# Kernel optimization log

Hardware: AMD Instinct MI355X
Metric: run time of the kernel (lower is better)

Reference implementation:

```python
import jax, jax.numpy as jnp
import numpy as np

EPS = 1e-5

def layer_norm(x, g, b):
    mu = jnp.mean(x, axis=-1, keepdims=True)
    var = jnp.var(x, axis=-1, keepdims=True)
    return (x - mu) * jax.lax.rsqrt(var + EPS) * g + b

def setup_inputs() -> dict:
    key = jax.random.key(0)
    ks = jax.random.split(key, 12)
    B, N, D, H = 32, 577, 768, 12
    Dh = D // H
    hid = 4 * D
    s = lambda d: 1.0 / np.sqrt(d)
    return {
        "x": jax.random.normal(ks[0], (B, N, D), jnp.float32),
        "ln1_g": jnp.ones((D,), jnp.float32),
        "ln1_b": jnp.zeros((D,), jnp.float32),
        "ln2_g": jnp.ones((D,), jnp.float32),
        "ln2_b": jnp.zeros((D,), jnp.float32),
        "w_qkv": jax.random.normal(ks[1], (D, 3 * D), jnp.float32) * s(D),
        "b_qkv": jnp.zeros((3 * D,), jnp.float32),
        "w_proj": jax.random.normal(ks[2], (D, D), jnp.float32) * s(D),
        "b_proj": jnp.zeros((D,), jnp.float32),
        "w_fc1": jax.random.normal(ks[3], (D, hid), jnp.float32) * s(D),
        "b_fc1": jnp.zeros((hid,), jnp.float32),
        "w_fc2": jax.random.normal(ks[4], (hid, D), jnp.float32) * s(hid),
        "b_fc2": jnp.zeros((D,), jnp.float32),
    }

def reference(x, ln1_g, ln1_b, ln2_g, ln2_b, w_qkv, b_qkv, w_proj, b_proj,
              w_fc1, b_fc1, w_fc2, b_fc2):
    B, N, D = x.shape
    H = 12
    Dh = D // H
    scale = Dh ** -0.5
    # --- attention branch ---
    h = layer_norm(x, ln1_g, ln1_b)
    qkv = h @ w_qkv + b_qkv                      # [B, N, 3D]
    qkv = qkv.reshape(B, N, 3, H, Dh).transpose(2, 0, 3, 1, 4)  # [3, B, H, N, Dh]
    q, k, v = qkv[0], qkv[1], qkv[2]
    attn = jnp.einsum('bhnd,bhmd->bhnm', q, k) * scale  # [B, H, N, N]
    attn = jax.nn.softmax(attn, axis=-1)
    o = jnp.einsum('bhnm,bhmd->bhnd', attn, v)           # [B, H, N, Dh]
    o = o.transpose(0, 2, 1, 3).reshape(B, N, D)
    o = o @ w_proj + b_proj
    x = x + o
    # --- MLP branch ---
    h = layer_norm(x, ln2_g, ln2_b)
    h = jnp.clip(h @ w_fc1 + b_fc1, 0.0, 6.0)            # ReLU6
    h = h @ w_fc2 + b_fc2
    return x + h
```

## Files before the change

kernel.cpp:

```cpp
#include <hip/hip_runtime.h>
#include <math.h>


typedef unsigned short u16;
typedef _Float16 f16;
typedef __attribute__((ext_vector_type(8))) _Float16 f16x8;
typedef __attribute__((ext_vector_type(4))) float f32x4;

__device__ __forceinline__ u16 f2h(float x) {
    union { f16 h; u16 u; } cv;
    cv.h = (f16)x;
    return cv.u;
}
__device__ __forceinline__ float h2f(u16 b) {
    union { u16 u; f16 h; } cv;
    cv.u = b;
    return (float)cv.h;
}
__device__ __forceinline__ void load_lds16(const u16* g, void* l) {
    __builtin_amdgcn_global_load_lds(
        (const __attribute__((address_space(1))) void*)g,
        (__attribute__((address_space(3))) void*)l, 16, 0, 0);
}
__device__ __forceinline__ int xcd_swz(int lid, int nwg) {
    const int x = lid & 7, pos = lid >> 3;
    const int q = nwg >> 3, r = nwg & 7;
    return (x < r ? x * (q + 1) : r * (q + 1) + (x - r) * q) + pos;
}

__global__ __launch_bounds__(256)
void wprep_kernel(const float* __restrict__ W, u16* __restrict__ Th,
                  int K, int N)
{
    __shared__ float t[32][33];
    const int n0 = blockIdx.x * 32, k0 = blockIdx.y * 32;
    const int tr = threadIdx.x >> 3, tc4 = (threadIdx.x & 7) * 4;
    const float4 v = *(const float4*)&W[(size_t)(k0 + tr) * N + n0 + tc4];
    t[tr][tc4 + 0] = v.x; t[tr][tc4 + 1] = v.y;
    t[tr][tc4 + 2] = v.z; t[tr][tc4 + 3] = v.w;
    __syncthreads();
    ushort4 h;
    h.x = f2h(t[tc4 + 0][tr]);
    h.y = f2h(t[tc4 + 1][tr]);
    h.z = f2h(t[tc4 + 2][tr]);
    h.w = f2h(t[tc4 + 3][tr]);
    *(ushort4*)&Th[(size_t)(n0 + tr) * K + k0 + tc4] = h;
}

__global__ __launch_bounds__(256)
void ln_kernel(const float* __restrict__ x, const float* __restrict__ g,
               const float* __restrict__ beta, u16* __restrict__ oh)
{
    const int row = blockIdx.x;
    const int tid = threadIdx.x;
    const float* xr = x + (size_t)row * 768;
    const float v0 = xr[tid], v1 = xr[tid + 256], v2 = xr[tid + 512];
    float s  = v0 + v1 + v2;
    float ss = v0 * v0 + v1 * v1 + v2 * v2;
    #pragma unroll
    for (int off = 1; off < 64; off <<= 1) {
        s  += __shfl_xor(s, off);
        ss += __shfl_xor(ss, off);
    }
    __shared__ float redS[4], redQ[4];
    const int wid = tid >> 6;
    if ((tid & 63) == 0) { redS[wid] = s; redQ[wid] = ss; }
    __syncthreads();
    s  = redS[0] + redS[1] + redS[2] + redS[3];
    ss = redQ[0] + redQ[1] + redQ[2] + redQ[3];
    const float mean = s * (1.0f / 768.0f);
    const float var  = ss * (1.0f / 768.0f) - mean * mean;
    const float rstd = rsqrtf(var + 1e-5f);
    u16* ohr = oh + (size_t)row * 768;
    #pragma unroll
    for (int u = 0; u < 3; ++u) {
        const int c = tid + u * 256;
        const float vv = (u == 0) ? v0 : (u == 1) ? v1 : v2;
        ohr[c] = f2h((vv - mean) * rstd * g[c] + beta[c]);
    }
}

template<int RELU6, int RES, int OMODE>
__global__ __launch_bounds__(256)
void mfma_gemm(const u16* __restrict__ Ah, const u16* __restrict__ Bh,
               const float* __restrict__ bias, const float* res,
               float* Cf, u16* __restrict__ Ch,
               u16* __restrict__ Qh_, u16* __restrict__ Kh_,
               u16* __restrict__ Vth_,
               int M, int N, int K)
{
    constexpr int LDSN = (OMODE == 2) ? 17408 : 16384;
    __shared__ u16 lds[LDSN];

    const int tid  = threadIdx.x;
    const int wave = tid >> 6;
    const int lane = tid & 63;

    const int nwg = gridDim.x * gridDim.y;
    int lid = blockIdx.y * gridDim.x + blockIdx.x;
    lid = xcd_swz(lid, nwg);
    const int bm = (lid / gridDim.x) * 128;
    const int bn = (lid % gridDim.x) * 128;

    const int r0 = wave * 16 + (lane >> 2);
    const int r1 = 64 + r0;
    const int c  = lane & 3;
    const int kg0 = c ^ ((r0 >> 1) & 3);
    const int kg1 = c ^ ((r1 >> 1) & 3);

    const u16* pA0 = Ah + (size_t)(bm + r0) * K + 8 * kg0;
    const u16* pA1 = Ah + (size_t)(bm + r1) * K + 8 * kg1;
    const u16* pB0 = Bh + (size_t)(bn + r0) * K + 8 * kg0;
    const u16* pB1 = Bh + (size_t)(bn + r1) * K + 8 * kg1;

    char* ldsb = (char*)lds;
    char* dA0 = ldsb +     0 + wave * 1024;
    char* dA1 = ldsb +  4096 + wave * 1024;
    char* dB0 = ldsb +  8192 + wave * 1024;
    char* dB1 = ldsb + 12288 + wave * 1024;

    const int am0 = (wave >> 1) * 64;
    const int bn0 = (wave & 1) * 64;
    const int l15 = lane & 15;
    const int lg  = lane >> 4;

    f32x4 acc[4][4] = {};
    const int nk = K >> 5;

    load_lds16(pA0, dA0); load_lds16(pA1, dA1);
    load_lds16(pB0, dB0); load_lds16(pB1, dB1);
    pA0 += 32; pA1 += 32; pB0 += 32; pB1 += 32;
    __syncthreads();

    int cur = 0;
    for (int ks = 0; ks < nk; ++ks) {
        if (ks + 1 < nk) {
            const int o = (cur ^ 1) << 14;
            load_lds16(pA0, dA0 + o); load_lds16(pA1, dA1 + o);
            load_lds16(pB0, dB0 + o); load_lds16(pB1, dB1 + o);
            pA0 += 32; pA1 += 32; pB0 += 32; pB1 += 32;
        }
        const u16* sA = lds + (cur << 13);
        const u16* sB = sA + 4096;

        f16x8 ah[4];
        #pragma unroll
        for (int fm = 0; fm < 4; ++fm) {
            const int ar = am0 + fm * 16 + l15;
            const int ph = (lg ^ ((ar >> 1) & 3)) * 8;
            ah[fm] = *(const f16x8*)&sA[ar * 32 + ph];
        }
        #pragma unroll
        for (int fn = 0; fn < 4; ++fn) {
            const int br = bn0 + fn * 16 + l15;
            const int ph = (lg ^ ((br >> 1) & 3)) * 8;
            const f16x8 bh = *(const f16x8*)&sB[br * 32 + ph];
            #pragma unroll
            for (int fm = 0; fm < 4; ++fm)
                acc[fm][fn] = __builtin_amdgcn_mfma_f32_16x16x32_f16(
                    ah[fm], bh, acc[fm][fn], 0, 0, 0);
        }
        __syncthreads();
        cur ^= 1;
    }

    if (OMODE == 2) {
        const int s  = bn / 768;
        const int hh = ((bn + bn0) - s * 768) >> 6;
        u16* eph = lds + wave * 4352;
        #pragma unroll
        for (int fn = 0; fn < 4; ++fn) {
            const float bv = bias[bn + bn0 + fn * 16 + l15];
            #pragma unroll
            for (int fm = 0; fm < 4; ++fm) {
                const f32x4 v = acc[fm][fn];
                #pragma unroll
                for (int j = 0; j < 4; ++j) {
                    const float o = v[j] + bv;
                    const int idx = (s == 2)
                        ? (fn * 16 + l15) * 68 + fm * 16 + lg * 4 + j
                        : (fm * 16 + lg * 4 + j) * 68 + fn * 16 + l15;
                    eph[idx] = f2h(o);
                }
            }
        }
        __syncthreads();
        if (s == 2) {
            const int r = bm + am0 + lane;
            const bool ok = r < M;
            const int b = (unsigned)r / 577u;
            const int n = r - b * 577;
            u16* dh = Vth_ + (size_t)(b * 12 + hh) * 64 * 640 + n;
            #pragma unroll 8
            for (int d = 0; d < 64; ++d) {
                const u16 vh = eph[d * 68 + lane];
                if (ok) dh[(size_t)d * 640] = vh;
            }
        } else {
            u16* base = (s == 0) ? Qh_ : Kh_;
            #pragma unroll 8
            for (int rr = 0; rr < 64; ++rr) {
                const int r = bm + am0 + rr;
                if (r < M) {
                    const int b = (unsigned)r / 577u;
                    const int n = r - b * 577;
                    base[((size_t)((b * 12 + hh) * 577 + n)) * 64 + lane] =
                        eph[rr * 68 + lane];
                }
            }
        }
    } else {
        #pragma unroll
        for (int fn = 0; fn < 4; ++fn) {
            const int cc = bn + bn0 + fn * 16 + l15;
            const float bv = bias[cc];
            #pragma unroll
            for (int fm = 0; fm < 4; ++fm) {
                const int rbase = bm + am0 + fm * 16 + lg * 4;
                const f32x4 v = acc[fm][fn];
                #pragma unroll
                for (int j = 0; j < 4; ++j) {
                    const int r = rbase + j;
                    if (r < M) {
                        float o = v[j] + bv;
                        if (RELU6) o = fminf(fmaxf(o, 0.0f), 6.0f);
                        if (RES)   o += res[(size_t)r * N + cc];
                        if (OMODE == 0) Cf[(size_t)r * N + cc] = o;
                        else            Ch[(size_t)r * N + cc] = f2h(o);
                    }
                }
            }
        }
    }
}

__global__ __launch_bounds__(256)
void attn_mfma(const u16* __restrict__ Qh, const u16* __restrict__ Kh,
               const u16* __restrict__ Vth, u16* __restrict__ Oh)
{
    constexpr int SEQ = 577, NP = 640;
    __shared__ u16 sK[2 * 4096], sV[2 * 4096];
    __shared__ u16 sPh[4][16 * 72];

    const int tid  = threadIdx.x;
    const int wave = tid >> 6;
    const int lane = tid & 63;
    const int l15 = lane & 15, lg = lane >> 4;

    const int nwg = gridDim.x * gridDim.y;
    int lid = blockIdx.y * gridDim.x + blockIdx.x;
    lid = xcd_swz(lid, nwg);
    const int q0 = (lid % gridDim.x) * 64;
    const int bh = lid / gridDim.x;

    const size_t qkBase = (size_t)bh * SEQ * 64;
    const size_t vBase  = (size_t)bh * 64 * NP;

    f16x8 qfh[2];
    {
        const size_t ro = qkBase + (size_t)(q0 + wave * 16 + l15) * 64;
        #pragma unroll
        for (int ks = 0; ks < 2; ++ks)
            qfh[ks] = *(const f16x8*)&Qh[ro + (ks * 4 + lg) * 8];
    }

    const int srow = lane >> 3;
    const int sc   = lane & 7;

    f32x4 oacc[4] = {};
    float mrun = -1e30f, lrun = 0.0f;
    constexpr int NT = 10;

    #pragma unroll
    for (int t = 0; t < 2; ++t) {
        const int row = wave * 16 + t * 8 + srow;
        const int lc  = sc ^ (row & 7);
        load_lds16(Kh + qkBase + (size_t)row * 64 + lc * 8,
                   (char*)sK + wave * 2048 + t * 1024);
        load_lds16(Vth + vBase + (size_t)row * NP + lc * 8,
                   (char*)sV + wave * 2048 + t * 1024);
    }
    __syncthreads();

    int cur = 0;
    for (int it = 0; it < NT; ++it) {
        const int kv0 = it * 64;
        if (it + 1 < NT) {
            const int nkv = kv0 + 64;
            const int o = (cur ^ 1) * 8192;
            #pragma unroll
            for (int t = 0; t < 2; ++t) {
                const int row = wave * 16 + t * 8 + srow;
                const int lc  = sc ^ (row & 7);
                load_lds16(Kh + qkBase + (size_t)(nkv + row) * 64 + lc * 8,
                           (char*)sK + o + wave * 2048 + t * 1024);
                load_lds16(Vth + vBase + (size_t)row * NP + nkv + lc * 8,
                           (char*)sV + o + wave * 2048 + t * 1024);
            }
        }
        const u16* sKc = sK + cur * 4096;
        const u16* sVc = sV + cur * 4096;

        f32x4 sacc[4] = {};
        __builtin_amdgcn_s_setprio(1);
        #pragma unroll
        for (int fkv = 0; fkv < 4; ++fkv) {
            const int row = fkv * 16 + l15;
            #pragma unroll
            for (int ks = 0; ks < 2; ++ks) {
                const int ph = ((ks * 4 + lg) ^ (row & 7)) * 8;
                const f16x8 kh = *(const f16x8*)&sKc[row * 64 + ph];
                sacc[fkv] = __builtin_amdgcn_mfma_f32_16x16x32_f16(
                    kh, qfh[ks], sacc[fkv], 0, 0, 0);
            }
        }
        __builtin_amdgcn_s_setprio(0);

        float p[4][4];
        float mt = -1e30f;
        const bool tail = (kv0 + 64 > SEQ);
        #pragma unroll
        for (int fkv = 0; fkv < 4; ++fkv)
            #pragma unroll
            for (int j = 0; j < 4; ++j) {
                float sv = sacc[fkv][j] * 0.125f;
                if (tail && (kv0 + fkv * 16 + lg * 4 + j >= SEQ)) sv = -1e30f;
                p[fkv][j] = sv;
                mt = fmaxf(mt, sv);
            }
        mt = fmaxf(mt, __shfl_xor(mt, 16));
        mt = fmaxf(mt, __shfl_xor(mt, 32));
        const float mnew = fmaxf(mrun, mt);
        const float corr = __expf(mrun - mnew);
        float rs = 0.0f;
        #pragma unroll
        for (int fkv = 0; fkv < 4; ++fkv)
            #pragma unroll
            for (int j = 0; j < 4; ++j) {
                p[fkv][j] = __expf(p[fkv][j] - mnew);
                rs += p[fkv][j];
            }
        rs += __shfl_xor(rs, 16);
        rs += __shfl_xor(rs, 32);
        lrun = lrun * corr + rs;
        mrun = mnew;
        #pragma unroll
        for (int fd = 0; fd < 4; ++fd)
            #pragma unroll
            for (int j = 0; j < 4; ++j) oacc[fd][j] *= corr;

        u16* phr = &sPh[wave][l15 * 72];
        #pragma unroll
        for (int fkv = 0; fkv < 4; ++fkv) {
            ushort4 hv;
            hv.x = f2h(p[fkv][0]);
            hv.y = f2h(p[fkv][1]);
            hv.z = f2h(p[fkv][2]);
            hv.w = f2h(p[fkv][3]);
            *(ushort4*)&phr[fkv * 16 + lg * 4] = hv;
        }

        __builtin_amdgcn_s_setprio(1);
        #pragma unroll
        for (int ks = 0; ks < 2; ++ks) {
            const f16x8 pbh = *(const f16x8*)&sPh[wave][l15 * 72 + (ks * 4 + lg) * 8];
            #pragma unroll
            for (int fd = 0; fd < 4; ++fd) {
                const int row = fd * 16 + l15;
                const int ph = ((ks * 4 + lg) ^ (row & 7)) * 8;
                const f16x8 vh = *(const f16x8*)&sVc[row * 64 + ph];
                oacc[fd] = __builtin_amdgcn_mfma_f32_16x16x32_f16(
                    vh, pbh, oacc[fd], 0, 0, 0);
            }
        }
        __builtin_amdgcn_s_setprio(0);

        __syncthreads();
        cur ^= 1;
    }

    const int q = q0 + wave * 16 + l15;
    if (q < SEQ) {
        const float inv = 1.0f / lrun;
        const int b = bh / 12, h = bh % 12;
        const size_t rowo = ((size_t)b * SEQ + q) * 768 + h * 64;
        #pragma unroll
        for (int fd = 0; fd < 4; ++fd) {
            ushort4 hv;
            hv.x = f2h(oacc[fd][0] * inv);
            hv.y = f2h(oacc[fd][1] * inv);
            hv.z = f2h(oacc[fd][2] * inv);
            hv.w = f2h(oacc[fd][3] * inv);
            *(ushort4*)&Oh[rowo + fd * 16 + lg * 4] = hv;
        }
    }
}

extern "C" void kernel_launch(void* const* d_in, const int* in_sizes, int n_in,
                              void* d_out, int out_size, void* d_ws, size_t ws_size,
                              hipStream_t stream)
{
    const float* x      = (const float*)d_in[0];
    const float* ln1_g  = (const float*)d_in[1];
    const float* ln1_b  = (const float*)d_in[2];
    const float* ln2_g  = (const float*)d_in[3];
    const float* ln2_b  = (const float*)d_in[4];
    const float* w_qkv  = (const float*)d_in[5];
    const float* b_qkv  = (const float*)d_in[6];
    const float* w_proj = (const float*)d_in[7];
    const float* b_proj = (const float*)d_in[8];
    const float* w_fc1  = (const float*)d_in[9];
    const float* b_fc1  = (const float*)d_in[10];
    const float* w_fc2  = (const float*)d_in[11];
    const float* b_fc2  = (const float*)d_in[12];
    float* out = (float*)d_out;

    const int M  = 18464;
    const int Mp = 18560;

    char* p = (char*)d_ws;
    u16* Wqkv  = (u16*)p;    p += (size_t)2304 * 768 * 2;
    u16* Wproj = (u16*)p;    p += (size_t)768 * 768 * 2;
    u16* Wfc1  = (u16*)p;    p += (size_t)3072 * 768 * 2;
    u16* Wfc2  = (u16*)p;    p += (size_t)768 * 3072 * 2;
    u16* A_h = (u16*)p;      p += (size_t)Mp * 768 * 2;
    const size_t QKB = ((size_t)384 * 577 * 64 + 8192) * 2;
    u16* Qh = (u16*)p;       p += QKB;
    u16* Kh = (u16*)p;       p += QKB;
    u16* Vth = (u16*)p;      p += (size_t)384 * 64 * 640 * 2;
    u16* fc1h = (u16*)p;     p += (size_t)Mp * 3072 * 2;

    wprep_kernel<<<dim3(72, 24),  256, 0, stream>>>(w_qkv,  Wqkv,  768, 2304);
    wprep_kernel<<<dim3(24, 24),  256, 0, stream>>>(w_proj, Wproj, 768, 768);
    wprep_kernel<<<dim3(96, 24),  256, 0, stream>>>(w_fc1,  Wfc1,  768, 3072);
    wprep_kernel<<<dim3(24, 96),  256, 0, stream>>>(w_fc2,  Wfc2,  3072, 768);

    ln_kernel<<<M, 256, 0, stream>>>(x, ln1_g, ln1_b, A_h);
    mfma_gemm<0, 0, 2><<<dim3(18, 145), 256, 0, stream>>>(
        A_h, Wqkv, b_qkv, nullptr, nullptr, nullptr,
        Qh, Kh, Vth, M, 2304, 768);
    attn_mfma<<<dim3(10, 384), 256, 0, stream>>>(Qh, Kh, Vth, A_h);
    mfma_gemm<0, 1, 0><<<dim3(6, 145), 256, 0, stream>>>(
        A_h, Wproj, b_proj, x, out, nullptr,
        nullptr, nullptr, nullptr, M, 768, 768);
    ln_kernel<<<M, 256, 0, stream>>>(out, ln2_g, ln2_b, A_h);
    mfma_gemm<1, 0, 1><<<dim3(24, 145), 256, 0, stream>>>(
        A_h, Wfc1, b_fc1, nullptr, nullptr, fc1h,
        nullptr, nullptr, nullptr, M, 3072, 768);
    mfma_gemm<0, 1, 0><<<dim3(6, 145), 256, 0, stream>>>(
        fc1h, Wfc2, b_fc2, out, out, nullptr,
        nullptr, nullptr, nullptr, M, 768, 3072);
}
```

Measured before the change: 677.3 us.

## Double K-step per stage in MFMA GEMM with 64-wide LDS tiles

The GEMM main loop now stages 64 K-elements per iteration instead of 32, split into two 32-wide LDS planes with an extra swizzle bit selecting the plane. It doubles LDS to 64KB and uses one explicit vmcnt wait plus barrier per stage, halving the barrier count per K. The intent is to cut synchronization overhead and give each wave more MFMA work between waits. The cost is doubled LDS usage, which may reduce occupancy per CU.

```diff
diff --git a/kernel.cpp b/kernel.cpp
--- a/kernel.cpp
+++ b/kernel.cpp
@@ -89,8 +89,7 @@
                u16* __restrict__ Vth_,
                int M, int N, int K)
 {
-    constexpr int LDSN = (OMODE == 2) ? 17408 : 16384;
-    __shared__ u16 lds[LDSN];
+    __shared__ u16 lds[32768];
 
     const int tid  = threadIdx.x;
     const int wave = tid >> 6;
@@ -102,22 +101,31 @@
     const int bm = (lid / gridDim.x) * 128;
     const int bn = (lid % gridDim.x) * 128;
 
-    const int r0 = wave * 16 + (lane >> 2);
+    const int rl = lane >> 2;
+    const int c  = lane & 3;
+    const int r0 = wave * 16 + rl;
     const int r1 = 64 + r0;
-    const int c  = lane & 3;
-    const int kg0 = c ^ ((r0 >> 1) & 3);
-    const int kg1 = c ^ ((r1 >> 1) & 3);
-
-    const u16* pA0 = Ah + (size_t)(bm + r0) * K + 8 * kg0;
-    const u16* pA1 = Ah + (size_t)(bm + r1) * K + 8 * kg1;
-    const u16* pB0 = Bh + (size_t)(bn + r0) * K + 8 * kg0;
-    const u16* pB1 = Bh + (size_t)(bn + r1) * K + 8 * kg1;
+    const int kgA0 = (((r0 >> 3) & 1) << 2) | (c ^ ((r0 >> 1) & 3));
+    const int kgA1 = (((r1 >> 3) & 1) << 2) | (c ^ ((r1 >> 1) & 3));
+
+    const u16* pA00 = Ah + (size_t)(bm + r0) * K + kgA0 * 8;
+    const u16* pA01 = Ah + (size_t)(bm + r0) * K + (kgA0 ^ 4) * 8;
+    const u16* pA10 = Ah + (size_t)(bm + r1) * K + kgA1 * 8;
+    const u16* pA11 = Ah + (size_t)(bm + r1) * K + (kgA1 ^ 4) * 8;
+    const u16* pB00 = Bh + (size_t)(bn + r0) * K + kgA0 * 8;
+    const u16* pB01 = Bh + (size_t)(bn + r0) * K + (kgA0 ^ 4) * 8;
+    const u16* pB10 = Bh + (size_t)(bn + r1) * K + kgA1 * 8;
+    const u16* pB11 = Bh + (size_t)(bn + r1) * K + (kgA1 ^ 4) * 8;
 
     char* ldsb = (char*)lds;
-    char* dA0 = ldsb +     0 + wave * 1024;
-    char* dA1 = ldsb +  4096 + wave * 1024;
-    char* dB0 = ldsb +  8192 + wave * 1024;
-    char* dB1 = ldsb + 12288 + wave * 1024;
+    char* dA00 = ldsb +     0 + wave * 1024;
+    char* dA01 = ldsb +  8192 + wave * 1024;
+    char* dA10 = ldsb +  4096 + wave * 1024;
+    char* dA11 = ldsb + 12288 + wave * 1024;
+    char* dB00 = ldsb + 16384 + wave * 1024;
+    char* dB01 = ldsb + 24576 + wave * 1024;
+    char* dB10 = ldsb + 20480 + wave * 1024;
+    char* dB11 = ldsb + 28672 + wave * 1024;
 
     const int am0 = (wave >> 1) * 64;
     const int bn0 = (wave & 1) * 64;
@@ -125,46 +133,60 @@
     const int lg  = lane >> 4;
 
     f32x4 acc[4][4] = {};
-    const int nk = K >> 5;
-
-    load_lds16(pA0, dA0); load_lds16(pA1, dA1);
-    load_lds16(pB0, dB0); load_lds16(pB1, dB1);
-    pA0 += 32; pA1 += 32; pB0 += 32; pB1 += 32;
-    __syncthreads();
+    const int np = K >> 6;
+
+    load_lds16(pA00, dA00); load_lds16(pA01, dA01);
+    load_lds16(pA10, dA10); load_lds16(pA11, dA11);
+    load_lds16(pB00, dB00); load_lds16(pB01, dB01);
+    load_lds16(pB10, dB10); load_lds16(pB11, dB11);
+    pA00 += 64; pA01 += 64; pA10 += 64; pA11 += 64;
+    pB00 += 64; pB01 += 64; pB10 += 64; pB11 += 64;
 
     int cur = 0;
-    for (int ks = 0; ks < nk; ++ks) {
-        if (ks + 1 < nk) {
-            const int o = (cur ^ 1) << 14;
-            load_lds16(pA0, dA0 + o); load_lds16(pA1, dA1 + o);
-            load_lds16(pB0, dB0 + o); load_lds16(pB1, dB1 + o);
-            pA0 += 32; pA1 += 32; pB0 += 32; pB1 += 32;
-        }
-        const u16* sA = lds + (cur << 13);
-        const u16* sB = sA + 4096;
-
-        f16x8 ah[4];
-        #pragma unroll
-        for (int fm = 0; fm < 4; ++fm) {
-            const int ar = am0 + fm * 16 + l15;
-            const int ph = (lg ^ ((ar >> 1) & 3)) * 8;
-            ah[fm] = *(const f16x8*)&sA[ar * 32 + ph];
-        }
-        #pragma unroll
-        for (int fn = 0; fn < 4; ++fn) {
-            const int br = bn0 + fn * 16 + l15;
-            const int ph = (lg ^ ((br >> 1) & 3)) * 8;
-            const f16x8 bh = *(const f16x8*)&sB[br * 32 + ph];
-            #pragma unroll
-            for (int fm = 0; fm < 4; ++fm)
-                acc[fm][fn] = __builtin_amdgcn_mfma_f32_16x16x32_f16(
-                    ah[fm], bh, acc[fm][fn], 0, 0, 0);
-        }
+    for (int p = 0; p < np; ++p) {
+        asm volatile("s_waitcnt vmcnt(0)" ::: "memory");
+        __builtin_amdgcn_s_barrier();
+        if (p + 1 < np) {
+            const int o = (cur ^ 1) << 15;
+            load_lds16(pA00, dA00 + o); load_lds16(pA01, dA01 + o);
+            load_lds16(pA10, dA10 + o); load_lds16(pA11, dA11 + o);
+            load_lds16(pB00, dB00 + o); load_lds16(pB01, dB01 + o);
+            load_lds16(pB10, dB10 + o); load_lds16(pB11, dB11 + o);
+            pA00 += 64; pA01 += 64; pA10 += 64; pA11 += 64;
+            pB00 += 64; pB01 += 64; pB10 += 64; pB11 += 64;
+        }
+        const u16* sA = lds + (cur << 14);
+        const u16* sB = sA + 8192;
+
+        #pragma unroll
+        for (int ss = 0; ss < 2; ++ss) {
+            f16x8 ah[4];
+            #pragma unroll
+            for (int fm = 0; fm < 4; ++fm) {
+                const int ar = am0 + fm * 16 + l15;
+                const int kg = ss * 4 + lg;
+                const int pc = (kg & 3) ^ ((ar >> 1) & 3);
+                const int pt = (kg >> 2) ^ ((ar >> 3) & 1);
+                ah[fm] = *(const f16x8*)&sA[pt * 4096 + ar * 32 + pc * 8];
+            }
+            #pragma unroll
+            for (int fn = 0; fn < 4; ++fn) {
+                const int br = bn0 + fn * 16 + l15;
+                const int kg = ss * 4 + lg;
+                const int pc = (kg & 3) ^ ((br >> 1) & 3);
+                const int pt = (kg >> 2) ^ ((br >> 3) & 1);
+                const f16x8 bh = *(const f16x8*)&sB[pt * 4096 + br * 32 + pc * 8];
+                #pragma unroll
+                for (int fm = 0; fm < 4; ++fm)
+                    acc[fm][fn] = __builtin_amdgcn_mfma_f32_16x16x32_f16(
+                        ah[fm], bh, acc[fm][fn], 0, 0, 0);
+            }
+        }
+        cur ^= 1;
+    }
+
+    if (OMODE == 2) {
         __syncthreads();
-        cur ^= 1;
-    }
-
-    if (OMODE == 2) {
         const int s  = bn / 768;
         const int hh = ((bn + bn0) - s * 768) >> 6;
         u16* eph = lds + wave * 4352;
```

Result: faster. 616.9 us (-8.9%).
